# Performance work log

Measured on AMD Instinct MI355X. Metric: run time of the kernel, lower is better.

## Reference

```python
import jax, jax.numpy as jnp
import numpy as np


def setup_inputs() -> dict:
    key = jax.random.key(0)
    x = jax.random.normal(key, (16, 2048, 64), dtype=jnp.float32)
    return {"x": x, "pred_len": 720, "k": 16, "low_freq": 1}


def reference(x, pred_len, k, low_freq):
    # x: (b, t, d); t assumed even (matches torch branch x_freq[:, low_freq:-1])
    b, t, d = x.shape
    x_freq = jnp.fft.rfft(x, axis=1)[:, low_freq:-1]          # (b, F, d) complex
    f = jnp.fft.rfftfreq(t).astype(jnp.float32)[low_freq:-1]  # (F,)

    # top-k frequencies per (batch, channel) by magnitude
    mag = jnp.transpose(jnp.abs(x_freq), (0, 2, 1))           # (b, d, F)
    _, idx = jax.lax.top_k(mag, k)                            # (b, d, k)
    xf_sel = jnp.take_along_axis(jnp.transpose(x_freq, (0, 2, 1)), idx, axis=2)
    xf_sel = jnp.transpose(xf_sel, (0, 2, 1))                 # (b, k, d)
    f_sel = jnp.transpose(f[idx], (0, 2, 1))                  # (b, k, d)

    # extrapolate: append conjugate / negated-frequency pairs
    xf = jnp.concatenate([xf_sel, jnp.conj(xf_sel)], axis=1)  # (b, 2k, d)
    ff = jnp.concatenate([f_sel, -f_sel], axis=1)[:, :, None, :]   # (b, 2k, 1, d)
    t_val = jnp.arange(t + pred_len, dtype=jnp.float32)[None, None, :, None]
    amp = (jnp.abs(xf) / t)[:, :, None, :]                    # (b, 2k, 1, d)
    phase = jnp.angle(xf)[:, :, None, :]                      # (b, 2k, 1, d)
    x_time = amp * jnp.cos(2.0 * jnp.pi * ff * t_val + phase) # (b, 2k, t+pred_len, d)
    return x_time.sum(axis=1)                                 # (b, t+pred_len, d)
```

## Files before the change

### kernel.cpp

```cpp
#include <hip/hip_runtime.h>
#include <hip/hip_bf16.h>

#define B_SZ 16
#define T_SZ 2048
#define D_SZ 64
#define M_SZ 1024
#define K_SEL 16
#define TOUT 2768
#define TPT 16
#define TAUS_PER_BLOCK (4 * TPT)
#define NCHUNK ((TOUT + TAUS_PER_BLOCK - 1) / TAUS_PER_BLOCK)

__global__ __launch_bounds__(256) void fft_topk_kernel(
    const float* __restrict__ x,
    int* __restrict__ sel_j,
    float* __restrict__ sel_re,
    float* __restrict__ sel_im)
{
    __shared__ float a_re[M_SZ], a_im[M_SZ];
    __shared__ float tw_re[M_SZ / 2], tw_im[M_SZ / 2];
    __shared__ float X_re[M_SZ], X_im[M_SZ];
    __shared__ float mag2[M_SZ];
    __shared__ float cand_v[64];
    __shared__ int   cand_j[64];

    const int bd   = blockIdx.x;
    const int b    = bd >> 6;
    const int d    = bd & 63;
    const int tid  = threadIdx.x;
    const int lane = tid & 63;
    const int w    = tid >> 6;

    for (int k = tid; k < M_SZ / 2; k += 256) {
        float a = (float)k * (1.0f / 512.0f);
        tw_re[k] =  cospif(a);
        tw_im[k] = -sinpif(a);
    }

    const float* xb = x + (size_t)b * T_SZ * D_SZ + d;
    #pragma unroll
    for (int r = 0; r < 4; ++r) {
        int m = tid + 256 * r;
        float xe = xb[(2 * m) * D_SZ];
        float xo = xb[(2 * m + 1) * D_SZ];
        int pos = __brev((unsigned)m) >> 22;
        a_re[pos] = xe;
        a_im[pos] = xo;
    }
    __syncthreads();

    for (int s = 0; s < 10; ++s) {
        #pragma unroll 2
        for (int q = tid; q < M_SZ / 2; q += 256) {
            int half = 1 << s;
            int pos  = q & (half - 1);
            int i0   = ((q >> s) << (s + 1)) + pos;
            int i1   = i0 + half;
            int twi  = pos << (9 - s);
            float wr = tw_re[twi], wi = tw_im[twi];
            float br = a_re[i1],  bi = a_im[i1];
            float tr = fmaf(wr, br, -wi * bi);
            float ti = fmaf(wr, bi,  wi * br);
            float ar = a_re[i0],  ai = a_im[i0];
            a_re[i0] = ar + tr;  a_im[i0] = ai + ti;
            a_re[i1] = ar - tr;  a_im[i1] = ai - ti;
        }
        __syncthreads();
    }

    for (int j = tid; j < M_SZ; j += 256) {
        if (j == 0) {
            X_re[0] = 0.0f; X_im[0] = 0.0f; mag2[0] = -2.0f;
            continue;
        }
        int jc = M_SZ - j;
        float zr = a_re[j],  zi = a_im[j];
        float cr = a_re[jc], ci = a_im[jc];
        float er = 0.5f * (zr + cr), ei = 0.5f * (zi - ci);
        float ur = zr - cr,  vv = zi + ci;
        float orr = 0.5f * vv, oii = -0.5f * ur;
        float a  = (float)j * (1.0f / 1024.0f);
        float twr =  cospif(a);
        float twq = -sinpif(a);
        float xr = er + twr * orr - twq * oii;
        float xi = ei + twr * oii + twq * orr;
        X_re[j] = xr; X_im[j] = xi;
        mag2[j] = xr * xr + xi * xi;
    }
    __syncthreads();

    float v[4]; int jj[4];
    #pragma unroll
    for (int r = 0; r < 4; ++r) {
        jj[r] = w * 256 + r * 64 + lane;
        v[r]  = mag2[jj[r]];
    }
    float my_v = -3.0f; int my_j = 0;
    for (int it = 0; it < K_SEL; ++it) {
        float bv = -2.5f; int bj = 1 << 20;
        #pragma unroll
        for (int r = 0; r < 4; ++r)
            if (v[r] > bv) { bv = v[r]; bj = jj[r]; }
        #pragma unroll
        for (int off = 32; off; off >>= 1) {
            float ov = __shfl_xor(bv, off);
            int   oj = __shfl_xor(bj, off);
            if (ov > bv || (ov == bv && oj < bj)) { bv = ov; bj = oj; }
        }
        if (lane == it) { my_v = bv; my_j = bj; }
        #pragma unroll
        for (int r = 0; r < 4; ++r)
            if (jj[r] == bj) v[r] = -2.0f;
    }
    if (lane < K_SEL) { cand_v[w * K_SEL + lane] = my_v; cand_j[w * K_SEL + lane] = my_j; }
    __syncthreads();

    if (w == 0) {
        float cv = cand_v[lane]; int cj = cand_j[lane];
        int out_j = 0;
        for (int it = 0; it < K_SEL; ++it) {
            float rv = cv; int rj = cj;
            #pragma unroll
            for (int off = 32; off; off >>= 1) {
                float ov = __shfl_xor(rv, off);
                int   oj = __shfl_xor(rj, off);
                if (ov > rv || (ov == rv && oj < rj)) { rv = ov; rj = oj; }
            }
            if (lane == it) out_j = rj;
            if (cj == rj) cv = -2.0f;
        }
        if (lane < K_SEL) {
            int j = out_j;
            sel_j [bd * K_SEL + lane] = j;
            sel_re[bd * K_SEL + lane] = X_re[j];
            sel_im[bd * K_SEL + lane] = X_im[j];
        }
    }
}

__global__ __launch_bounds__(256) void synth_kernel(
    const int*   __restrict__ sel_j,
    const float* __restrict__ sel_re,
    const float* __restrict__ sel_im,
    float* __restrict__ out)
{
    const int bid   = blockIdx.x;
    const int b     = bid / NCHUNK;
    const int chunk = bid - b * NCHUNK;
    const int tid   = threadIdx.x;
    const int d     = tid & 63;
    const int tg    = tid >> 6;

    const int tau0 = chunk * TAUS_PER_BLOCK + tg * TPT;
    if (tau0 >= TOUT) return;
    const int nu = (TOUT - tau0 < TPT) ? (TOUT - tau0) : TPT;

    const int g = (b * D_SZ + d) * K_SEL;
    int   j [K_SEL];
    float re[K_SEL];
    float im[K_SEL];
    const int4*   pj = (const int4*)  (sel_j  + g);
    const float4* pr = (const float4*)(sel_re + g);
    const float4* pi = (const float4*)(sel_im + g);
    #pragma unroll
    for (int r = 0; r < 4; ++r) {
        int4   a = pj[r];
        float4 c = pr[r];
        float4 s = pi[r];
        j [4*r+0] = a.x; j [4*r+1] = a.y; j [4*r+2] = a.z; j [4*r+3] = a.w;
        re[4*r+0] = c.x; re[4*r+1] = c.y; re[4*r+2] = c.z; re[4*r+3] = c.w;
        im[4*r+0] = s.x; im[4*r+1] = s.y; im[4*r+2] = s.z; im[4*r+3] = s.w;
    }

    float acc[TPT];
    #pragma unroll
    for (int u = 0; u < TPT; ++u) acc[u] = 0.0f;

    #pragma unroll
    for (int q = 0; q < K_SEL; ++q) {
        int   ph0 = (j[q] * tau0) & (T_SZ - 1);
        float r0  = (float)ph0  * (1.0f / (float)T_SZ);
        float rw  = (float)j[q] * (1.0f / (float)T_SZ);
        float c   = __builtin_amdgcn_cosf(r0);
        float s   = __builtin_amdgcn_sinf(r0);
        float cw  = __builtin_amdgcn_cosf(rw);
        float sw  = __builtin_amdgcn_sinf(rw);
        #pragma unroll
        for (int u = 0; u < TPT; ++u) {
            acc[u] = fmaf(re[q], c, acc[u]);
            acc[u] = fmaf(-im[q], s, acc[u]);
            float cn = fmaf(c, cw, -s * sw);
            float sn = fmaf(s, cw,  c * sw);
            c = cn; s = sn;
        }
    }

    float* ob = out + ((size_t)b * TOUT + tau0) * D_SZ + d;
    #pragma unroll
    for (int u = 0; u < TPT; ++u) {
        if (u < nu) ob[(size_t)u * D_SZ] = acc[u] * (1.0f / 1024.0f);
    }
}

extern "C" void kernel_launch(void* const* d_in, const int* in_sizes, int n_in,
                              void* d_out, int out_size, void* d_ws, size_t ws_size,
                              hipStream_t stream) {
    const float* x = (const float*)d_in[0];

    int*   sel_j  = (int*)d_ws;
    float* sel_re = (float*)((char*)d_ws + (size_t)B_SZ * D_SZ * K_SEL * 4);
    float* sel_im = (float*)((char*)d_ws + (size_t)2 * B_SZ * D_SZ * K_SEL * 4);

    fft_topk_kernel<<<dim3(B_SZ * D_SZ), dim3(256), 0, stream>>>(
        x, sel_j, sel_re, sel_im);

    synth_kernel<<<dim3(B_SZ * NCHUNK), dim3(256), 0, stream>>>(
        sel_j, sel_re, sel_im, (float*)d_out);
}
```

Baseline: 110.0 us.

## Replace radix-2 FFT with radix-4 digit-reversed FFT and in-place split stage

Replaces the 10-stage radix-2 in-shared-memory FFT with a 5-stage radix-4 FFT. Input is gathered in base-4 digit-reversed order and the first stage is done with float4 shared-memory accesses. This halves the number of barrier-separated passes and LDS round trips. The real-FFT split step now handles each conjugate pair in one thread and writes results in place, which drops the separate X arrays and cuts the shared-memory footprint. Risks are a larger twiddle table and possible LDS bank conflicts in the radix-4 strides.

```diff
diff --git a/kernel.cpp b/kernel.cpp
--- a/kernel.cpp
+++ b/kernel.cpp
@@ -11,15 +11,19 @@
 #define TAUS_PER_BLOCK (4 * TPT)
 #define NCHUNK ((TOUT + TAUS_PER_BLOCK - 1) / TAUS_PER_BLOCK)
 
+__device__ __forceinline__ int digitrev4(int m) {
+    int v = __brev((unsigned)m) >> 22;
+    return ((v & 0x155) << 1) | ((v >> 1) & 0x155);
+}
+
 __global__ __launch_bounds__(256) void fft_topk_kernel(
     const float* __restrict__ x,
     int* __restrict__ sel_j,
     float* __restrict__ sel_re,
     float* __restrict__ sel_im)
 {
-    __shared__ float a_re[M_SZ], a_im[M_SZ];
-    __shared__ float tw_re[M_SZ / 2], tw_im[M_SZ / 2];
-    __shared__ float X_re[M_SZ], X_im[M_SZ];
+    __shared__ __align__(16) float a_re[M_SZ], a_im[M_SZ];
+    __shared__ float tw_re[768], tw_im[768];
     __shared__ float mag2[M_SZ];
     __shared__ float cand_v[64];
     __shared__ int   cand_j[64];
@@ -31,61 +35,100 @@
     const int lane = tid & 63;
     const int w    = tid >> 6;
 
-    for (int k = tid; k < M_SZ / 2; k += 256) {
+    const float* xb = x + (size_t)b * T_SZ * D_SZ + d;
+    float xe[4], xo[4];
+    #pragma unroll
+    for (int r = 0; r < 4; ++r) {
+        int pos = tid + 256 * r;
+        int m   = digitrev4(pos);
+        xe[r] = xb[(2 * m) * D_SZ];
+        xo[r] = xb[(2 * m + 1) * D_SZ];
+    }
+
+    for (int k = tid; k < 768; k += 256) {
         float a = (float)k * (1.0f / 512.0f);
         tw_re[k] =  cospif(a);
         tw_im[k] = -sinpif(a);
     }
 
-    const float* xb = x + (size_t)b * T_SZ * D_SZ + d;
-    #pragma unroll
-    for (int r = 0; r < 4; ++r) {
-        int m = tid + 256 * r;
-        float xe = xb[(2 * m) * D_SZ];
-        float xo = xb[(2 * m + 1) * D_SZ];
-        int pos = __brev((unsigned)m) >> 22;
-        a_re[pos] = xe;
-        a_im[pos] = xo;
-    }
-    __syncthreads();
-
-    for (int s = 0; s < 10; ++s) {
-        #pragma unroll 2
-        for (int q = tid; q < M_SZ / 2; q += 256) {
-            int half = 1 << s;
-            int pos  = q & (half - 1);
-            int i0   = ((q >> s) << (s + 1)) + pos;
-            int i1   = i0 + half;
-            int twi  = pos << (9 - s);
-            float wr = tw_re[twi], wi = tw_im[twi];
-            float br = a_re[i1],  bi = a_im[i1];
-            float tr = fmaf(wr, br, -wi * bi);
-            float ti = fmaf(wr, bi,  wi * br);
-            float ar = a_re[i0],  ai = a_im[i0];
-            a_re[i0] = ar + tr;  a_im[i0] = ai + ti;
-            a_re[i1] = ar - tr;  a_im[i1] = ai - ti;
-        }
+    #pragma unroll
+    for (int r = 0; r < 4; ++r) {
+        int pos = tid + 256 * r;
+        a_re[pos] = xe[r];
+        a_im[pos] = xo[r];
+    }
+    __syncthreads();
+
+    {
+        float4* pr4 = reinterpret_cast<float4*>(a_re);
+        float4* pi4 = reinterpret_cast<float4*>(a_im);
+        float4 vr = pr4[tid];
+        float4 vi = pi4[tid];
+        float t0r = vr.x + vr.z, t0i = vi.x + vi.z;
+        float t1r = vr.x - vr.z, t1i = vi.x - vi.z;
+        float t2r = vr.y + vr.w, t2i = vi.y + vi.w;
+        float t3r = vr.y - vr.w, t3i = vi.y - vi.w;
+        vr.x = t0r + t2r;  vi.x = t0i + t2i;
+        vr.y = t1r + t3i;  vi.y = t1i - t3r;
+        vr.z = t0r - t2r;  vi.z = t0i - t2i;
+        vr.w = t1r - t3i;  vi.w = t1i + t3r;
+        pr4[tid] = vr;
+        pi4[tid] = vi;
+    }
+    __syncthreads();
+
+    #pragma unroll
+    for (int s = 1; s < 5; ++s) {
+        const int q   = 1 << (2 * s);
+        const int pos = tid & (q - 1);
+        const int i0  = ((tid >> (2 * s)) << (2 * s + 2)) + pos;
+        const int e   = pos << (8 - 2 * s);
+
+        float w1r = tw_re[e],     w1i = tw_im[e];
+        float w2r = tw_re[2 * e], w2i = tw_im[2 * e];
+        float w3r = tw_re[3 * e], w3i = tw_im[3 * e];
+
+        float b0r = a_re[i0],         b0i = a_im[i0];
+        float u1r = a_re[i0 + q],     u1i = a_im[i0 + q];
+        float u2r = a_re[i0 + 2 * q], u2i = a_im[i0 + 2 * q];
+        float u3r = a_re[i0 + 3 * q], u3i = a_im[i0 + 3 * q];
+
+        float b1r = fmaf(w1r, u1r, -w1i * u1i), b1i = fmaf(w1r, u1i, w1i * u1r);
+        float b2r = fmaf(w2r, u2r, -w2i * u2i), b2i = fmaf(w2r, u2i, w2i * u2r);
+        float b3r = fmaf(w3r, u3r, -w3i * u3i), b3i = fmaf(w3r, u3i, w3i * u3r);
+
+        float t0r = b0r + b2r, t0i = b0i + b2i;
+        float t1r = b0r - b2r, t1i = b0i - b2i;
+        float t2r = b1r + b3r, t2i = b1i + b3i;
+        float t3r = b1r - b3r, t3i = b1i - b3i;
+
+        a_re[i0]         = t0r + t2r;  a_im[i0]         = t0i + t2i;
+        a_re[i0 + q]     = t1r + t3i;  a_im[i0 + q]     = t1i - t3r;
+        a_re[i0 + 2 * q] = t0r - t2r;  a_im[i0 + 2 * q] = t0i - t2i;
+        a_re[i0 + 3 * q] = t1r - t3i;  a_im[i0 + 3 * q] = t1i + t3r;
         __syncthreads();
     }
 
-    for (int j = tid; j < M_SZ; j += 256) {
-        if (j == 0) {
-            X_re[0] = 0.0f; X_im[0] = 0.0f; mag2[0] = -2.0f;
-            continue;
-        }
+    if (tid == 0) { mag2[0] = -2.0f; }
+    #pragma unroll
+    for (int r = 0; r < 2; ++r) {
+        int j  = 1 + tid + 256 * r;
         int jc = M_SZ - j;
         float zr = a_re[j],  zi = a_im[j];
         float cr = a_re[jc], ci = a_im[jc];
-        float er = 0.5f * (zr + cr), ei = 0.5f * (zi - ci);
-        float ur = zr - cr,  vv = zi + ci;
-        float orr = 0.5f * vv, oii = -0.5f * ur;
-        float a  = (float)j * (1.0f / 1024.0f);
-        float twr =  cospif(a);
-        float twq = -sinpif(a);
-        float xr = er + twr * orr - twq * oii;
-        float xi = ei + twr * oii + twq * orr;
-        X_re[j] = xr; X_im[j] = xi;
-        mag2[j] = xr * xr + xi * xi;
+        float er  = 0.5f * (zr + cr), ei = 0.5f * (zi - ci);
+        float orr = 0.5f * (zi + ci), oii = -0.5f * (zr - cr);
+        float ang = (float)j * (1.0f / 1024.0f);
+        float twr =  cospif(ang);
+        float twq = -sinpif(ang);
+        float pr_ = fmaf(twr, orr, -twq * oii);
+        float pi_ = fmaf(twr, oii,  twq * orr);
+        float xjr = er + pr_, xji = ei + pi_;
+        float xcr = er - pr_, xci = -(ei - pi_);
+        a_re[j]  = xjr;  a_im[j]  = xji;
+        a_re[jc] = xcr;  a_im[jc] = xci;
+        mag2[j]  = xjr * xjr + xji * xji;
+        mag2[jc] = xcr * xcr + xci * xci;
     }
     __syncthreads();
 
@@ -132,8 +175,8 @@
         if (lane < K_SEL) {
             int j = out_j;
             sel_j [bd * K_SEL + lane] = j;
-            sel_re[bd * K_SEL + lane] = X_re[j];
-            sel_im[bd * K_SEL + lane] = X_im[j];
+            sel_re[bd * K_SEL + lane] = a_re[j];
+            sel_im[bd * K_SEL + lane] = a_im[j];
         }
     }
 }
```

Result: faster. 107.2 us (-2.6%).
